# Kernel tuning notes

Hardware: AMD Instinct MI355X
Metric: run time of the kernel (lower is better)

Reference implementation:

```python
import jax, jax.numpy as jnp
import numpy as np

N_NODES = 100000
N_EDGES = 3200000
HID = 32
HEADS = 2
EDGE_IN = 4
NEG_SLOPE = 0.2  # PyG GATConv default


def gat_conv(x, src, dst, W, att_src, att_dst, bias, heads, out_ch, concat):
    """PyG-style GATConv with self-loops already included in (src, dst).
    x: [N, in], W: [in, heads*out_ch], att_*: [heads, out_ch], bias: [heads*out_ch] or [out_ch]."""
    N = x.shape[0]
    h = (x @ W).reshape(N, heads, out_ch)                      # [N,H,C]
    a_src = jnp.einsum('nhc,hc->nh', h, att_src)               # [N,H]
    a_dst = jnp.einsum('nhc,hc->nh', h, att_dst)
    e = a_src[src] + a_dst[dst]                                # [E,H]
    e = jnp.where(e > 0, e, NEG_SLOPE * e)                     # leaky_relu
    # segment softmax over incoming edges of each dst node
    m = jax.ops.segment_max(e, dst, num_segments=N)            # [N,H]
    ex = jnp.exp(e - m[dst])
    s = jax.ops.segment_sum(ex, dst, num_segments=N)
    alpha = ex / (s[dst] + 1e-16)                              # [E,H]
    msg = h[src] * alpha[:, :, None]                           # [E,H,C]
    out = jax.ops.segment_sum(msg, dst, num_segments=N)        # [N,H,C]
    out = out.reshape(N, heads * out_ch) if concat else out.mean(axis=1)
    return out + bias


def setup_inputs() -> dict:
    key = jax.random.key(0)
    ks = jax.random.split(key, 16)
    x = jax.random.normal(ks[0], (N_NODES, 1), dtype=jnp.float32)
    edge_index = jax.random.randint(ks[1], (2, N_EDGES), 0, N_NODES, dtype=jnp.int32)
    edge_attr = jax.random.uniform(ks[2], (N_EDGES, EDGE_IN), dtype=jnp.float32)
    g = lambda k, shape, fan: (jax.random.normal(k, shape, dtype=jnp.float32) / np.sqrt(fan)).astype(jnp.float32)
    params = {
        'W1': g(ks[3], (1, HEADS * HID), 1),
        'att_src1': g(ks[4], (HEADS, HID), HID),
        'att_dst1': g(ks[5], (HEADS, HID), HID),
        'b1': jnp.zeros((HEADS * HID,), jnp.float32),
        'W2': g(ks[6], (HEADS * HID, HID), HEADS * HID),
        'att_src2': g(ks[7], (1, HID), HID),
        'att_dst2': g(ks[8], (1, HID), HID),
        'b2': jnp.zeros((HID,), jnp.float32),
        'Wm1': g(ks[9], (2 * HID + EDGE_IN, 32), 2 * HID + EDGE_IN),
        'bm1': jnp.zeros((32,), jnp.float32),
        'Wm2': g(ks[10], (32, 16), 32),
        'bm2': jnp.zeros((16,), jnp.float32),
        'Wm3': g(ks[11], (16, 1), 16),
        'bm3': jnp.zeros((1,), jnp.float32),
    }
    return {'x': x, 'edge_index': edge_index, 'edge_attr': edge_attr, **params}


def reference(x, edge_index, edge_attr, W1, att_src1, att_dst1, b1, W2, att_src2, att_dst2, b2,
              Wm1, bm1, Wm2, bm2, Wm3, bm3):
    N = x.shape[0]
    # PyG GATConv adds self-loops by default
    loop = jnp.arange(N, dtype=edge_index.dtype)
    src = jnp.concatenate([edge_index[0], loop])
    dst = jnp.concatenate([edge_index[1], loop])
    out = gat_conv(x, src, dst, W1, att_src1, att_dst1, b1, HEADS, HID, concat=True)
    out = jax.nn.relu(out)
    node_embs = gat_conv(out, src, dst, W2, att_src2, att_dst2, b2, 1, HID, concat=False)  # [N,HID]
    # edge scorer on ORIGINAL edges (no self-loops)
    e_src, e_dst = edge_index[0], edge_index[1]
    feat = jnp.concatenate([node_embs[e_src], node_embs[e_dst], edge_attr], axis=1)  # [E, 2*HID+4]
    h = jax.nn.relu(feat @ Wm1 + bm1)   # dropout is identity in eval mode
    h = jax.nn.relu(h @ Wm2 + bm2)
    scores = jax.nn.sigmoid(h @ Wm3 + bm3)
    return scores.squeeze(-1)
```

## Files before the change

kernel.cpp:

```cpp
#include <hip/hip_runtime.h>
#include <math.h>

#define NN 100000
#define NE 3200000
#define NEG 0.2f
#define NBKT 391
#define TILE_E 8192
#define BCAP 12288
#define K6_BLOCKS 3125

typedef __attribute__((ext_vector_type(8))) short bf16x8;
typedef __attribute__((ext_vector_type(4))) float f32x4;

__device__ __forceinline__ float leaky(float v) { return v > 0.f ? v : NEG * v; }

__device__ __forceinline__ unsigned int f2bf(float f) {
    unsigned int u = __float_as_uint(f);
    return (u + 0x7fffu + ((u >> 16) & 1u)) >> 16;
}
__device__ __forceinline__ float bf2f(unsigned short h) {
    return __uint_as_float(((unsigned int)h) << 16);
}

__global__ void __launch_bounds__(256) kA1_part(const int* __restrict__ ei,
                                                int* __restrict__ bktcnt,
                                                int* __restrict__ ebuf) {
    __shared__ int cnt[NBKT];
    __shared__ int cur[NBKT];
    int t = threadIdx.x;
    for (int i = t; i < NBKT; i += 256) cnt[i] = 0;
    __syncthreads();
    int base = blockIdx.x * TILE_E;
    int m = min(TILE_E, NE - base);
    int tq = m >> 10;
    const int4* d4 = (const int4*)(ei + NE + base);
    const int4* s4 = (const int4*)(ei + base);
    int4 dd[8];
#pragma unroll
    for (int q = 0; q < 8; ++q) {
        if (q < tq) {
            int4 v = d4[q * 256 + t];
            dd[q] = v;
            atomicAdd(&cnt[v.x >> 8], 1);
            atomicAdd(&cnt[v.y >> 8], 1);
            atomicAdd(&cnt[v.z >> 8], 1);
            atomicAdd(&cnt[v.w >> 8], 1);
        }
    }
    __syncthreads();
    for (int i = t; i < NBKT; i += 256) {
        int c = cnt[i];
        cur[i] = c ? atomicAdd(&bktcnt[i], c) : 0;
    }
    __syncthreads();
#pragma unroll
    for (int q = 0; q < 8; ++q) {
        if (q < tq) {
            int4 sv = s4[q * 256 + t];
            int4 dv = dd[q];
            int b, p;
            b = dv.x >> 8; p = atomicAdd(&cur[b], 1);
            if (p < BCAP) ebuf[b * BCAP + p] = (sv.x << 8) | (dv.x & 255);
            b = dv.y >> 8; p = atomicAdd(&cur[b], 1);
            if (p < BCAP) ebuf[b * BCAP + p] = (sv.y << 8) | (dv.y & 255);
            b = dv.z >> 8; p = atomicAdd(&cur[b], 1);
            if (p < BCAP) ebuf[b * BCAP + p] = (sv.z << 8) | (dv.z & 255);
            b = dv.w >> 8; p = atomicAdd(&cur[b], 1);
            if (p < BCAP) ebuf[b * BCAP + p] = (sv.w << 8) | (dv.w & 255);
        }
    }
}

__global__ void __launch_bounds__(512) kscan(const int* __restrict__ bktcnt,
                                             int* __restrict__ bktoff,
                                             int* __restrict__ rowst,
                                             const float* __restrict__ W1,
                                             const float* __restrict__ as1,
                                             const float* __restrict__ ad1,
                                             float* __restrict__ c4) {
    int t = threadIdx.x;
    if (t < 2) {
        float cs = 0.f, cd = 0.f;
        for (int c = 0; c < 32; ++c) {
            float w = W1[t * 32 + c];
            cs += w * as1[t * 32 + c];
            cd += w * ad1[t * 32 + c];
        }
        c4[t] = cs;
        c4[2 + t] = cd;
    }
    __shared__ int sh[512];
    int v = (t < NBKT) ? min(bktcnt[t], BCAP) : 0;
    sh[t] = v;
    __syncthreads();
    for (int o = 1; o < 512; o <<= 1) {
        int add = (t >= o) ? sh[t - o] : 0;
        __syncthreads();
        sh[t] += add;
        __syncthreads();
    }
    if (t < NBKT) bktoff[t] = sh[t] - v;
    if (t == 511) {
        bktoff[NBKT] = sh[511];
        rowst[NN] = sh[511];
    }
}

__global__ void __launch_bounds__(256) kB_sort(const int* __restrict__ bktcnt,
                                               const int* __restrict__ bktoff,
                                               const int* __restrict__ ebuf,
                                               int* __restrict__ rowst,
                                               int* __restrict__ srcidx) {
    __shared__ int cnt[256];
    __shared__ int tmp[256];
    int b = blockIdx.x, t = threadIdx.x;
    int n = min(bktcnt[b], BCAP);
    int obase = bktoff[b];
    const int* ib = ebuf + b * BCAP;
    const int4* ib4 = (const int4*)ib;
    int nq = n >> 2;
    cnt[t] = 0;
    __syncthreads();
    for (int i = t; i < nq; i += 256) {
        int4 v = ib4[i];
        atomicAdd(&cnt[v.x & 255], 1);
        atomicAdd(&cnt[v.y & 255], 1);
        atomicAdd(&cnt[v.z & 255], 1);
        atomicAdd(&cnt[v.w & 255], 1);
    }
    for (int i = (nq << 2) + t; i < n; i += 256)
        atomicAdd(&cnt[ib[i] & 255], 1);
    __syncthreads();
    int v = cnt[t];
    tmp[t] = v;
    __syncthreads();
    for (int o = 1; o < 256; o <<= 1) {
        int add = (t >= o) ? tmp[t - o] : 0;
        __syncthreads();
        tmp[t] += add;
        __syncthreads();
    }
    int excl = tmp[t] - v;
    int node = (b << 8) + t;
    if (node < NN) rowst[node] = obase + excl;
    cnt[t] = obase + excl;
    __syncthreads();
    for (int i = t; i < nq; i += 256) {
        int4 e4 = ib4[i];
        int p;
        p = atomicAdd(&cnt[e4.x & 255], 1); srcidx[p] = e4.x >> 8;
        p = atomicAdd(&cnt[e4.y & 255], 1); srcidx[p] = e4.y >> 8;
        p = atomicAdd(&cnt[e4.z & 255], 1); srcidx[p] = e4.z >> 8;
        p = atomicAdd(&cnt[e4.w & 255], 1); srcidx[p] = e4.w >> 8;
    }
    for (int i = (nq << 2) + t; i < n; i += 256) {
        int e = ib[i];
        int p = atomicAdd(&cnt[e & 255], 1);
        srcidx[p] = e >> 8;
    }
}

__global__ void __launch_bounds__(256) k_agg1(const int* __restrict__ rowstart,
                                              const int* __restrict__ srcidx,
                                              const float* __restrict__ x,
                                              const float* __restrict__ c4,
                                              float2* __restrict__ r2) {
    int gtid = blockIdx.x * blockDim.x + threadIdx.x;
    int n = gtid >> 4;
    int lane = gtid & 15;
    if (n >= NN) return;
    float c0 = c4[0], c1 = c4[1], c2 = c4[2], c3 = c4[3];
    float xd = x[n];
    float xdc2 = xd * c2, xdc3 = xd * c3;
    float s0 = 0.f, s1 = 0.f, t0 = 0.f, t1 = 0.f;
    int rs = rowstart[n], re = rowstart[n + 1];
    for (int i = rs + lane; i < re; i += 16) {
        float xs = x[__builtin_nontemporal_load(srcidx + i)];
        float ex0 = __expf(leaky(xs * c0 + xdc2));
        float ex1 = __expf(leaky(xs * c1 + xdc3));
        s0 += ex0;
        s1 += ex1;
        t0 += ex0 * xs;
        t1 += ex1 * xs;
    }
#pragma unroll
    for (int m = 8; m >= 1; m >>= 1) {
        s0 += __shfl_xor(s0, m, 16);
        s1 += __shfl_xor(s1, m, 16);
        t0 += __shfl_xor(t0, m, 16);
        t1 += __shfl_xor(t1, m, 16);
    }
    if (lane == 0) {
        float ex0 = __expf(leaky(xd * (c0 + c2)));
        float ex1 = __expf(leaky(xd * (c1 + c3)));
        s0 += ex0;
        s1 += ex1;
        t0 += ex0 * xd;
        t1 += ex1 * xd;
        r2[n] = make_float2(t0 / (s0 + 1e-16f), t1 / (s1 + 1e-16f));
    }
}

__global__ void __launch_bounds__(256) k3_node(const float2* __restrict__ r2,
                                               const float* __restrict__ W1,
                                               const float* __restrict__ b1,
                                               const float* __restrict__ W2,
                                               const float* __restrict__ as2,
                                               const float* __restrict__ ad2,
                                               unsigned int* __restrict__ h8,
                                               float2* __restrict__ a2) {
    int n = blockIdx.x * blockDim.x + threadIdx.x;
    if (n >= NN) return;
    float2 r = r2[n];
    float h2[32];
#pragma unroll
    for (int c = 0; c < 32; ++c) h2[c] = 0.f;
    for (int j = 0; j < 64; ++j) {
        float o = W1[j] * (j < 32 ? r.x : r.y) + b1[j];
        o = fmaxf(o, 0.f);
#pragma unroll
        for (int c = 0; c < 32; ++c) h2[c] += o * W2[j * 32 + c];
    }
    float asum = 0.f, adsum = 0.f;
#pragma unroll
    for (int c = 0; c < 32; ++c) {
        asum += h2[c] * as2[c];
        adsum += h2[c] * ad2[c];
    }
    a2[n] = make_float2(asum, adsum);
    unsigned int w[8];
#pragma unroll
    for (int q = 0; q < 8; ++q) {
        int v = __builtin_amdgcn_cvt_pk_fp8_f32(h2[q * 4 + 0], h2[q * 4 + 1], 0, false);
        v = __builtin_amdgcn_cvt_pk_fp8_f32(h2[q * 4 + 2], h2[q * 4 + 3], v, true);
        w[q] = (unsigned int)v;
    }
    uint4* hg = (uint4*)(h8 + (size_t)n * 8);
    hg[0] = make_uint4(w[0], w[1], w[2], w[3]);
    hg[1] = make_uint4(w[4], w[5], w[6], w[7]);
}

__global__ void __launch_bounds__(256) k_agg2(const int* __restrict__ rowstart,
                                              const int* __restrict__ srcidx,
                                              const unsigned char* __restrict__ h8,
                                              const float2* __restrict__ a2,
                                              const float* __restrict__ b2,
                                              unsigned short* __restrict__ embq) {
    __shared__ int loff[256];
    __shared__ float lex[256];
    int tid = threadIdx.x;
    int gtid = blockIdx.x * 256 + tid;
    int n = gtid >> 5;
    int c = gtid & 31;
    if (n >= NN) return;
    int wbase = tid & ~31;
    float2 an = a2[n];
    float adn = an.y;
    float exn = __expf(leaky(an.x + adn));
    float u = exn * __builtin_amdgcn_cvt_f32_fp8(h8[((unsigned)n << 5) + c], 0);
    float lsum = 0.f;
    int rs = rowstart[n], re = rowstart[n + 1];
    for (int base = rs; base < re; base += 32) {
        int cnt = re - base;
        int off = 0;
        float exj = 0.f;
        if (c < cnt) {
            int sjv = __builtin_nontemporal_load(srcidx + base + c);
            off = sjv << 5;
            float2 asrc = a2[sjv];
            exj = __expf(leaky(asrc.x + adn));
            lsum += exj;
        }
        loff[tid] = off;
        asm volatile("s_waitcnt lgkmcnt(0)" ::: "memory");
        int4 ov[8];
#pragma unroll
        for (int q = 0; q < 8; ++q) ov[q] = ((const int4*)(loff + wbase))[q];
        unsigned int hb[32];
#pragma unroll
        for (int q = 0; q < 8; ++q) {
            hb[4 * q + 0] = h8[ov[q].x + c];
            hb[4 * q + 1] = h8[ov[q].y + c];
            hb[4 * q + 2] = h8[ov[q].z + c];
            hb[4 * q + 3] = h8[ov[q].w + c];
        }
        lex[tid] = exj;
        asm volatile("s_waitcnt lgkmcnt(0)" ::: "memory");
#pragma unroll
        for (int q = 0; q < 8; ++q) {
            float4 ev = ((const float4*)(lex + wbase))[q];
            u += ev.x * __builtin_amdgcn_cvt_f32_fp8(hb[4 * q + 0], 0);
            u += ev.y * __builtin_amdgcn_cvt_f32_fp8(hb[4 * q + 1], 0);
            u += ev.z * __builtin_amdgcn_cvt_f32_fp8(hb[4 * q + 2], 0);
            u += ev.w * __builtin_amdgcn_cvt_f32_fp8(hb[4 * q + 3], 0);
        }
    }
#pragma unroll
    for (int m = 16; m >= 1; m >>= 1) lsum += __shfl_xor(lsum, m, 32);
    float ssum = lsum + exn;
    embq[((unsigned)n << 5) + c] = (unsigned short)f2bf(u / (ssum + 1e-16f) + b2[c]);
}

__global__ void __launch_bounds__(256) k6_mfma(const int* __restrict__ ei,
                                               const float* __restrict__ ea,
                                               const unsigned short* __restrict__ embq,
                                               const float* __restrict__ Wm1,
                                               const float* __restrict__ bm1,
                                               const float* __restrict__ Wm2,
                                               const float* __restrict__ bm2,
                                               const float* __restrict__ Wm3,
                                               const float* __restrict__ bm3,
                                               float* __restrict__ out) {
    __shared__ unsigned short ldsq[4][4 * 640];
    int tid = threadIdx.x;
    int wave = tid >> 6, lane = tid & 63;
    int m = lane & 15, quad = lane >> 4;
    unsigned short* wl = ldsq[wave];
    float* wz = (float*)wl;

    bf16x8 B1[3][2];
#pragma unroll
    for (int c = 0; c < 3; ++c) {
#pragma unroll
        for (int t = 0; t < 2; ++t) {
            bf16x8 v;
#pragma unroll
            for (int j = 0; j < 8; ++j) {
                int kk = c * 32 + quad * 8 + j;
                float w = (kk < 68) ? Wm1[kk * 32 + 2 * m + t] : 0.f;
                v[j] = (short)f2bf(w);
            }
            B1[c][t] = v;
        }
    }
    bf16x8 B2;
#pragma unroll
    for (int j = 0; j < 8; ++j)
        B2[j] = (short)f2bf(Wm2[(quad * 8 + j) * 16 + m]);
    float bl = bm1[2 * m], bh = bm1[2 * m + 1];
    float b2v = bm2[m], w3v = Wm3[m], b3 = bm3[0];

    int gw = blockIdx.x * 4 + wave;

    int s2[2][4], d2[2][4];
    f32x4 ev2[2][4];
    bf16x8 A0[2][4], A1[2][4];

    auto LOADIDX = [&](int b, int ii) {
#pragma unroll
        for (int u = 0; u < 4; ++u) {
            int e = (gw * 16 + ii * 4) * 16 + u * 16 + m;
            s2[b][u] = __builtin_nontemporal_load(ei + e);
            d2[b][u] = __builtin_nontemporal_load(ei + NE + e);
            if (quad == 0)
                ev2[b][u] = __builtin_nontemporal_load((const f32x4*)ea + e);
        }
    };
    auto GATHER = [&](int b) {
#pragma unroll
        for (int u = 0; u < 4; ++u) {
            A0[b][u] = *(const bf16x8*)(embq + (((unsigned)s2[b][u] << 5) + quad * 8));
            A1[b][u] = *(const bf16x8*)(embq + (((unsigned)d2[b][u] << 5) + quad * 8));
        }
    };

    LOADIDX(0, 0);
    GATHER(0);
    LOADIDX(1, 1);

#pragma unroll
    for (int ii = 0; ii < 4; ++ii) {
        const int b = ii & 1;
        int eb0 = (gw * 16 + ii * 4) * 16;
#pragma unroll
        for (int u = 0; u < 4; ++u) {
            bf16x8 z = {0, 0, 0, 0, 0, 0, 0, 0};
            if (quad == 0) {
                f32x4 av = ev2[b][u];
                z[0] = (short)f2bf(av[0]);
                z[1] = (short)f2bf(av[1]);
                z[2] = (short)f2bf(av[2]);
                z[3] = (short)f2bf(av[3]);
            }
            f32x4 accL = {bl, bl, bl, bl};
            f32x4 accH = {bh, bh, bh, bh};
            accL = __builtin_amdgcn_mfma_f32_16x16x32_bf16(A0[b][u], B1[0][0], accL, 0, 0, 0);
            accH = __builtin_amdgcn_mfma_f32_16x16x32_bf16(A0[b][u], B1[0][1], accH, 0, 0, 0);
            accL = __builtin_amdgcn_mfma_f32_16x16x32_bf16(A1[b][u], B1[1][0], accL, 0, 0, 0);
            accH = __builtin_amdgcn_mfma_f32_16x16x32_bf16(A1[b][u], B1[1][1], accH, 0, 0, 0);
            accL = __builtin_amdgcn_mfma_f32_16x16x32_bf16(z, B1[2][0], accL, 0, 0, 0);
            accH = __builtin_amdgcn_mfma_f32_16x16x32_bf16(z, B1[2][1], accH, 0, 0, 0);
#pragma unroll
            for (int r = 0; r < 4; ++r) {
                int row = quad * 4 + r;
                unsigned int uL = __float_as_uint(fmaxf(accL[r], 0.f)) + 0x8000u;
                unsigned int uH = __float_as_uint(fmaxf(accH[r], 0.f)) + 0x8000u;
                unsigned int packed = __builtin_amdgcn_perm(uH, uL, 0x07060302);
                *(unsigned int*)(wl + u * 640 + row * 40 + 2 * m) = packed;
            }
        }
        if (ii < 3) GATHER(b ^ 1);
        if (ii < 2) LOADIDX(b, ii + 2);
        asm volatile("s_waitcnt lgkmcnt(0)" ::: "memory");
#pragma unroll
        for (int u = 0; u < 4; ++u) {
            bf16x8 aq = *(const bf16x8*)(wl + u * 640 + m * 40 + quad * 8);
            f32x4 accO = {b2v, b2v, b2v, b2v};
            accO = __builtin_amdgcn_mfma_f32_16x16x32_bf16(aq, B2, accO, 0, 0, 0);
#pragma unroll
            for (int r = 0; r < 4; ++r) {
                int edge = u * 16 + quad * 4 + r;
                wz[edge * 20 + m] = fmaxf(accO[r], 0.f) * w3v;
            }
        }
        asm volatile("s_waitcnt lgkmcnt(0)" ::: "memory");
        {
            f32x4 p0 = *(const f32x4*)(wz + lane * 20 + 0);
            f32x4 p1 = *(const f32x4*)(wz + lane * 20 + 4);
            f32x4 p2 = *(const f32x4*)(wz + lane * 20 + 8);
            f32x4 p3 = *(const f32x4*)(wz + lane * 20 + 12);
            float sum = ((p0[0] + p0[1]) + (p0[2] + p0[3])) +
                        ((p1[0] + p1[1]) + (p1[2] + p1[3])) +
                        ((p2[0] + p2[1]) + (p2[2] + p2[3])) +
                        ((p3[0] + p3[1]) + (p3[2] + p3[3]));
            float sc = 1.f / (1.f + __expf(-(sum + b3)));
            __builtin_nontemporal_store(sc, out + eb0 + lane);
        }
        asm volatile("" ::: "memory");
    }
}

extern "C" void kernel_launch(void* const* d_in, const int* in_sizes, int n_in,
                              void* d_out, int out_size, void* d_ws, size_t ws_size,
                              hipStream_t stream) {
    const float* x   = (const float*)d_in[0];
    const int* ei    = (const int*)d_in[1];
    const float* ea  = (const float*)d_in[2];
    const float* W1  = (const float*)d_in[3];
    const float* as1 = (const float*)d_in[4];
    const float* ad1 = (const float*)d_in[5];
    const float* b1  = (const float*)d_in[6];
    const float* W2  = (const float*)d_in[7];
    const float* as2 = (const float*)d_in[8];
    const float* ad2 = (const float*)d_in[9];
    const float* b2  = (const float*)d_in[10];
    const float* Wm1 = (const float*)d_in[11];
    const float* bm1 = (const float*)d_in[12];
    const float* Wm2 = (const float*)d_in[13];
    const float* bm2 = (const float*)d_in[14];
    const float* Wm3 = (const float*)d_in[15];
    const float* bm3 = (const float*)d_in[16];
    float* out = (float*)d_out;

    char* ws = (char*)d_ws;
    float* c4      = (float*)(ws + 0);
    int*   bktcnt  = (int*)  (ws + 256);
    int*   bktoff  = (int*)  (ws + 2048);
    int*   rowst   = (int*)  (ws + 5632);
    float* r2      = (float*)(ws + 405760);
    float* a2      = (float*)(ws + 1205760);
    int*   ebufP   = (int*)  (ws + 2005760);
    int*   srcidx  = (int*)  (ws + 21224192);
    unsigned char* h8    = (unsigned char*)ebufP;
    unsigned short* embq = (unsigned short*)(ws + 34024192);

    const int NB = (NN + 255) / 256;
    const int TB = (NE + TILE_E - 1) / TILE_E;

    hipMemsetAsync(bktcnt, 0, NBKT * sizeof(int), stream);
    hipLaunchKernelGGL(kA1_part, dim3(TB), dim3(256), 0, stream, ei, bktcnt, ebufP);
    hipLaunchKernelGGL(kscan, dim3(1), dim3(512), 0, stream, bktcnt, bktoff, rowst,
                       W1, as1, ad1, c4);
    hipLaunchKernelGGL(kB_sort, dim3(NBKT), dim3(256), 0, stream, bktcnt, bktoff, ebufP,
                       rowst, srcidx);
    hipLaunchKernelGGL(k_agg1, dim3((NN * 16 + 255) / 256), dim3(256), 0, stream,
                       rowst, srcidx, x, c4, (float2*)r2);
    hipLaunchKernelGGL(k3_node, dim3(NB), dim3(256), 0, stream, (float2*)r2, W1, b1, W2,
                       as2, ad2, (unsigned int*)h8, (float2*)a2);
    hipLaunchKernelGGL(k_agg2, dim3((NN * 32 + 255) / 256), dim3(256), 0, stream,
                       rowst, srcidx, h8, (float2*)a2, b2, embq);
    hipLaunchKernelGGL(k6_mfma, dim3(K6_BLOCKS), dim3(256), 0, stream, ei, ea, embq,
                       Wm1, bm1, Wm2, bm2, Wm3, bm3, out);
}
```

Measured before the change: 360.0 us.

## Fuse layer-1 attention aggregation into bucket sort kernel via LDS atomics

```diff
diff --git a/kernel.cpp b/kernel.cpp
--- a/kernel.cpp
+++ b/kernel.cpp
@@ -110,16 +110,33 @@
                                                const int* __restrict__ bktoff,
                                                const int* __restrict__ ebuf,
                                                int* __restrict__ rowst,
-                                               int* __restrict__ srcidx) {
+                                               int* __restrict__ srcidx,
+                                               const float* __restrict__ x,
+                                               const float* __restrict__ c4,
+                                               float2* __restrict__ r2) {
     __shared__ int cnt[256];
     __shared__ int tmp[256];
+    __shared__ float lx[256];
+    __shared__ float s0a[256], s1a[256], t0a[256], t1a[256];
     int b = blockIdx.x, t = threadIdx.x;
     int n = min(bktcnt[b], BCAP);
     int obase = bktoff[b];
     const int* ib = ebuf + b * BCAP;
     const int4* ib4 = (const int4*)ib;
     int nq = n >> 2;
+    int node = (b << 8) + t;
+    float c0 = c4[0], c1 = c4[1], c2 = c4[2], c3 = c4[3];
+    float xd = (node < NN) ? x[node] : 0.f;
+    lx[t] = xd;
     cnt[t] = 0;
+    {
+        float e0 = __expf(leaky(xd * (c0 + c2)));
+        float e1 = __expf(leaky(xd * (c1 + c3)));
+        s0a[t] = e0;
+        s1a[t] = e1;
+        t0a[t] = e0 * xd;
+        t1a[t] = e1 * xd;
+    }
     __syncthreads();
     for (int i = t; i < nq; i += 256) {
         int4 v = ib4[i];
@@ -141,64 +158,57 @@
         __syncthreads();
     }
     int excl = tmp[t] - v;
-    int node = (b << 8) + t;
     if (node < NN) rowst[node] = obase + excl;
     cnt[t] = obase + excl;
     __syncthreads();
     for (int i = t; i < nq; i += 256) {
         int4 e4 = ib4[i];
-        int p;
-        p = atomicAdd(&cnt[e4.x & 255], 1); srcidx[p] = e4.x >> 8;
-        p = atomicAdd(&cnt[e4.y & 255], 1); srcidx[p] = e4.y >> 8;
-        p = atomicAdd(&cnt[e4.z & 255], 1); srcidx[p] = e4.z >> 8;
-        p = atomicAdd(&cnt[e4.w & 255], 1); srcidx[p] = e4.w >> 8;
+        int p, d, s;
+        float xs, xv, ex0, ex1;
+        d = e4.x & 255; s = e4.x >> 8;
+        p = atomicAdd(&cnt[d], 1); srcidx[p] = s;
+        xs = x[s]; xv = lx[d];
+        ex0 = __expf(leaky(xs * c0 + xv * c2));
+        ex1 = __expf(leaky(xs * c1 + xv * c3));
+        atomicAdd(&s0a[d], ex0); atomicAdd(&s1a[d], ex1);
+        atomicAdd(&t0a[d], ex0 * xs); atomicAdd(&t1a[d], ex1 * xs);
+        d = e4.y & 255; s = e4.y >> 8;
+        p = atomicAdd(&cnt[d], 1); srcidx[p] = s;
+        xs = x[s]; xv = lx[d];
+        ex0 = __expf(leaky(xs * c0 + xv * c2));
+        ex1 = __expf(leaky(xs * c1 + xv * c3));
+        atomicAdd(&s0a[d], ex0); atomicAdd(&s1a[d], ex1);
+        atomicAdd(&t0a[d], ex0 * xs); atomicAdd(&t1a[d], ex1 * xs);
+        d = e4.z & 255; s = e4.z >> 8;
+        p = atomicAdd(&cnt[d], 1); srcidx[p] = s;
+        xs = x[s]; xv = lx[d];
+        ex0 = __expf(leaky(xs * c0 + xv * c2));
+        ex1 = __expf(leaky(xs * c1 + xv * c3));
+        atomicAdd(&s0a[d], ex0); atomicAdd(&s1a[d], ex1);
+        atomicAdd(&t0a[d], ex0 * xs); atomicAdd(&t1a[d], ex1 * xs);
+        d = e4.w & 255; s = e4.w >> 8;
+        p = atomicAdd(&cnt[d], 1); srcidx[p] = s;
+        xs = x[s]; xv = lx[d];
+        ex0 = __expf(leaky(xs * c0 + xv * c2));
+        ex1 = __expf(leaky(xs * c1 + xv * c3));
+        atomicAdd(&s0a[d], ex0); atomicAdd(&s1a[d], ex1);
+        atomicAdd(&t0a[d], ex0 * xs); atomicAdd(&t1a[d], ex1 * xs);
     }
     for (int i = (nq << 2) + t; i < n; i += 256) {
         int e = ib[i];
-        int p = atomicAdd(&cnt[e & 255], 1);
-        srcidx[p] = e >> 8;
-    }
-}
-
-__global__ void __launch_bounds__(256) k_agg1(const int* __restrict__ rowstart,
-                                              const int* __restrict__ srcidx,
-                                              const float* __restrict__ x,
-                                              const float* __restrict__ c4,
-                                              float2* __restrict__ r2) {
-    int gtid = blockIdx.x * blockDim.x + threadIdx.x;
-    int n = gtid >> 4;
-    int lane = gtid & 15;
-    if (n >= NN) return;
-    float c0 = c4[0], c1 = c4[1], c2 = c4[2], c3 = c4[3];
-    float xd = x[n];
-    float xdc2 = xd * c2, xdc3 = xd * c3;
-    float s0 = 0.f, s1 = 0.f, t0 = 0.f, t1 = 0.f;
-    int rs = rowstart[n], re = rowstart[n + 1];
-    for (int i = rs + lane; i < re; i += 16) {
-        float xs = x[__builtin_nontemporal_load(srcidx + i)];
-        float ex0 = __expf(leaky(xs * c0 + xdc2));
-        float ex1 = __expf(leaky(xs * c1 + xdc3));
-        s0 += ex0;
-        s1 += ex1;
-        t0 += ex0 * xs;
-        t1 += ex1 * xs;
-    }
-#pragma unroll
-    for (int m = 8; m >= 1; m >>= 1) {
-        s0 += __shfl_xor(s0, m, 16);
-        s1 += __shfl_xor(s1, m, 16);
-        t0 += __shfl_xor(t0, m, 16);
-        t1 += __shfl_xor(t1, m, 16);
-    }
-    if (lane == 0) {
-        float ex0 = __expf(leaky(xd * (c0 + c2)));
-        float ex1 = __expf(leaky(xd * (c1 + c3)));
-        s0 += ex0;
-        s1 += ex1;
-        t0 += ex0 * xd;
-        t1 += ex1 * xd;
-        r2[n] = make_float2(t0 / (s0 + 1e-16f), t1 / (s1 + 1e-16f));
-    }
+        int d = e & 255, s = e >> 8;
+        int p = atomicAdd(&cnt[d], 1);
+        srcidx[p] = s;
+        float xs = x[s], xv = lx[d];
+        float ex0 = __expf(leaky(xs * c0 + xv * c2));
+        float ex1 = __expf(leaky(xs * c1 + xv * c3));
+        atomicAdd(&s0a[d], ex0); atomicAdd(&s1a[d], ex1);
+        atomicAdd(&t0a[d], ex0 * xs); atomicAdd(&t1a[d], ex1 * xs);
+    }
+    __syncthreads();
+    if (node < NN)
+        r2[node] = make_float2(t0a[t] / (s0a[t] + 1e-16f),
+                               t1a[t] / (s1a[t] + 1e-16f));
 }
 
 __global__ void __launch_bounds__(256) k3_node(const float2* __restrict__ r2,
@@ -472,8 +482,6 @@
     hipLaunchKernelGGL(kscan, dim3(1), dim3(512), 0, stream, bktcnt, bktoff, rowst,
                        W1, as1, ad1, c4);
     hipLaunchKernelGGL(kB_sort, dim3(NBKT), dim3(256), 0, stream, bktcnt, bktoff, ebufP,
-                       rowst, srcidx);
-    hipLaunchKernelGGL(k_agg1, dim3((NN * 16 + 255) / 256), dim3(256), 0, stream,
                        rowst, srcidx, x, c4, (float2*)r2);
     hipLaunchKernelGGL(k3_node, dim3(NB), dim3(256), 0, stream, (float2*)r2, W1, b1, W2,
                        as2, ad2, (unsigned int*)h8, (float2*)a2);
```

New measurement: 413.0 us. 14.7% more time.

## Stage bucketed edges in LDS before coalesced scatter to global buckets

Applied to the files above, without the earlier changes.

```diff
diff --git a/kernel.cpp b/kernel.cpp
--- a/kernel.cpp
+++ b/kernel.cpp
@@ -26,7 +26,12 @@
                                                 int* __restrict__ bktcnt,
                                                 int* __restrict__ ebuf) {
     __shared__ int cnt[NBKT];
+    __shared__ int eofs[NBKT];
     __shared__ int cur[NBKT];
+    __shared__ int lcur[NBKT];
+    __shared__ int sh[512];
+    __shared__ int lstage[TILE_E];
+    __shared__ unsigned short lbkt[TILE_E];
     int t = threadIdx.x;
     for (int i = t; i < NBKT; i += 256) cnt[i] = 0;
     __syncthreads();
@@ -48,8 +53,22 @@
         }
     }
     __syncthreads();
+    sh[t] = (t < NBKT) ? cnt[t] : 0;
+    sh[t + 256] = (t + 256 < NBKT) ? cnt[t + 256] : 0;
+    __syncthreads();
+    for (int o = 1; o < 512; o <<= 1) {
+        int a0 = (t >= o) ? sh[t - o] : 0;
+        int a1 = ((t + 256) >= o) ? sh[t + 256 - o] : 0;
+        __syncthreads();
+        sh[t] += a0;
+        sh[t + 256] += a1;
+        __syncthreads();
+    }
     for (int i = t; i < NBKT; i += 256) {
         int c = cnt[i];
+        int e = sh[i] - c;
+        eofs[i] = e;
+        lcur[i] = e;
         cur[i] = c ? atomicAdd(&bktcnt[i], c) : 0;
     }
     __syncthreads();
@@ -59,15 +78,21 @@
             int4 sv = s4[q * 256 + t];
             int4 dv = dd[q];
             int b, p;
-            b = dv.x >> 8; p = atomicAdd(&cur[b], 1);
-            if (p < BCAP) ebuf[b * BCAP + p] = (sv.x << 8) | (dv.x & 255);
-            b = dv.y >> 8; p = atomicAdd(&cur[b], 1);
-            if (p < BCAP) ebuf[b * BCAP + p] = (sv.y << 8) | (dv.y & 255);
-            b = dv.z >> 8; p = atomicAdd(&cur[b], 1);
-            if (p < BCAP) ebuf[b * BCAP + p] = (sv.z << 8) | (dv.z & 255);
-            b = dv.w >> 8; p = atomicAdd(&cur[b], 1);
-            if (p < BCAP) ebuf[b * BCAP + p] = (sv.w << 8) | (dv.w & 255);
-        }
+            b = dv.x >> 8; p = atomicAdd(&lcur[b], 1);
+            lstage[p] = (sv.x << 8) | (dv.x & 255); lbkt[p] = (unsigned short)b;
+            b = dv.y >> 8; p = atomicAdd(&lcur[b], 1);
+            lstage[p] = (sv.y << 8) | (dv.y & 255); lbkt[p] = (unsigned short)b;
+            b = dv.z >> 8; p = atomicAdd(&lcur[b], 1);
+            lstage[p] = (sv.z << 8) | (dv.z & 255); lbkt[p] = (unsigned short)b;
+            b = dv.w >> 8; p = atomicAdd(&lcur[b], 1);
+            lstage[p] = (sv.w << 8) | (dv.w & 255); lbkt[p] = (unsigned short)b;
+        }
+    }
+    __syncthreads();
+    for (int i = t; i < m; i += 256) {
+        int b = lbkt[i];
+        int p = cur[b] + (i - eofs[b]);
+        if (p < BCAP) ebuf[b * BCAP + p] = lstage[i];
     }
 }
 
```

New measurement: 345.4 us. -4.0%, faster.
